# Performance work log

Hardware: AMD Instinct MI355X
Metric: run time of the kernel (lower is better)

The kernel has to match this reference:

```python
import jax, jax.numpy as jnp
import numpy as np

HID = 768
HEADS = 12
HEAD_LEN = HID // HEADS
SCALE_INV = 1.0 / np.sqrt(HEAD_LEN).astype(np.float32)


def setup_inputs() -> dict:
    key = jax.random.key(0)
    ks = jax.random.split(key, 5)
    std = 1.0 / np.sqrt(HID)
    return {
        "x": jax.random.normal(ks[0], (1, 4096, HID), dtype=jnp.float32),
        "w_q": jax.random.normal(ks[1], (HID, HID), dtype=jnp.float32) * std,
        "w_k": jax.random.normal(ks[2], (HID, HID), dtype=jnp.float32) * std,
        "w_v": jax.random.normal(ks[3], (HID, HID), dtype=jnp.float32) * std,
        "w_fc": jax.random.normal(ks[4], (HID, HID), dtype=jnp.float32) * std,
    }


def reference(x, w_q, w_k, w_v, w_fc):
    B, S, D = x.shape
    # torch Linear weight layout [out, in]: y = x @ W.T
    def proj_heads(w):
        y = jnp.einsum("bsd,ed->bse", x, w)
        return y.reshape(B, S, HEADS, HEAD_LEN).transpose(0, 2, 1, 3)  # bhsd
    q = proj_heads(w_q)
    k = proj_heads(w_k)
    v = proj_heads(w_v)
    scores = SCALE_INV * jnp.einsum("bhqd,bhkd->bhqk", q, k)
    attn = jax.nn.softmax(scores, axis=-1)
    out = jnp.einsum("bhqk,bhkd->bhqd", attn, v)
    out = out.transpose(0, 2, 1, 3).reshape(B, S, D)
    return jnp.einsum("bsd,ed->bse", out, w_fc)
```

## Files before the change

kernel.cpp:

```cpp
#include <hip/hip_runtime.h>
#include <hip/hip_bf16.h>

#define S_LEN 4096
#define HID 768
#define NHEAD 12
#define HL 64
#define PSS 72
#define QB 128

typedef __attribute__((ext_vector_type(8))) short short8;
typedef __attribute__((ext_vector_type(4))) float f32x4;
using bf16 = __hip_bfloat16;

__device__ __forceinline__ void gl2lds16(const void* g, void* l) {
  __builtin_amdgcn_global_load_lds((__attribute__((address_space(1))) void*)(g),
                                   (__attribute__((address_space(3))) void*)(l),
                                   16, 0, 0);
}

__device__ __forceinline__ f32x4 mfma_bf16(short8 a, short8 b, f32x4 c) {
  return __builtin_amdgcn_mfma_f32_16x16x32_bf16(a, b, c, 0, 0, 0);
}

__device__ __forceinline__ void storeC(float* C, long idx, float v) { C[idx] = v; }
__device__ __forceinline__ void storeC(bf16* C, long idx, float v) { C[idx] = __float2bfloat16(v); }

#define BAR() asm volatile("s_waitcnt lgkmcnt(0)\n\ts_barrier" ::: "memory")

__global__ __launch_bounds__(256) void cvt_all(
    const float* __restrict__ x, const float* __restrict__ wq,
    const float* __restrict__ wk, const float* __restrict__ wv,
    const float* __restrict__ wfc, bf16* __restrict__ xb, bf16* __restrict__ wqb,
    bf16* __restrict__ wkb, bf16* __restrict__ wvb, bf16* __restrict__ wfcb) {
  const long NX = (long)S_LEN * HID;
  const long NW = (long)HID * HID;
  long i = ((long)blockIdx.x * 256 + threadIdx.x) * 4;
  const float* src;
  bf16* dst;
  long off;
  if (i < NX) {
    src = x; dst = xb; off = i;
  } else {
    long j = i - NX;
    int wsel = (int)(j / NW);
    off = j - (long)wsel * NW;
    src = wsel == 0 ? wq : wsel == 1 ? wk : wsel == 2 ? wv : wfc;
    dst = wsel == 0 ? wqb : wsel == 1 ? wkb : wsel == 2 ? wvb : wfcb;
  }
  float4 v = *(const float4*)(src + off);
  bf16 h0 = __float2bfloat16(v.x), h1 = __float2bfloat16(v.y);
  bf16 h2 = __float2bfloat16(v.z), h3 = __float2bfloat16(v.w);
  ushort4 o;
  o.x = *(unsigned short*)&h0; o.y = *(unsigned short*)&h1;
  o.z = *(unsigned short*)&h2; o.w = *(unsigned short*)&h3;
  *(ushort4*)(dst + off) = o;
}

template <typename OT>
__global__ __launch_bounds__(256) void gemm_bt(
    const bf16* __restrict__ A, const bf16* __restrict__ B0,
    const bf16* __restrict__ B1, const bf16* __restrict__ B2,
    OT* __restrict__ C0, OT* __restrict__ C1, OT* __restrict__ C2, float qscale) {
  constexpr int K = HID;
  __shared__ __align__(16) bf16 As[128 * 32];
  __shared__ __align__(16) bf16 Bs[128 * 32];
  const int z = blockIdx.z;
  const bf16* B = (z == 0) ? B0 : (z == 1) ? B1 : B2;
  OT* C = (z == 0) ? C0 : (z == 1) ? C1 : C2;
  const float sc = (z == 0) ? qscale : 1.0f;
  const int bm = blockIdx.y, bn = blockIdx.x;
  const int t = threadIdx.x, lane = t & 63, w = t >> 6;
  const int wm = w >> 1, wn = w & 1;
  const int q4 = lane >> 4, c16 = lane & 15;
  const int srow = lane >> 2, scol = (lane & 3) * 8;
  const bf16* Ab = A + (long)bm * 128 * K;
  const bf16* Bb = B + (long)bn * 128 * K;
  f32x4 acc[4][4] = {};
  for (int k0 = 0; k0 < K; k0 += 32) {
#pragma unroll
    for (int r = 0; r < 2; ++r) {
      int rowb = r * 64 + w * 16;
      gl2lds16(Ab + (long)(rowb + srow) * K + k0 + scol, &As[rowb * 32]);
      gl2lds16(Bb + (long)(rowb + srow) * K + k0 + scol, &Bs[rowb * 32]);
    }
    __syncthreads();
    short8 af[4], bfv[4];
#pragma unroll
    for (int i = 0; i < 4; ++i)
      af[i] = *(const short8*)&As[(wm * 64 + i * 16 + c16) * 32 + q4 * 8];
#pragma unroll
    for (int j = 0; j < 4; ++j)
      bfv[j] = *(const short8*)&Bs[(wn * 64 + j * 16 + c16) * 32 + q4 * 8];
#pragma unroll
    for (int i = 0; i < 4; ++i)
#pragma unroll
      for (int j = 0; j < 4; ++j)
        acc[i][j] = mfma_bf16(af[i], bfv[j], acc[i][j]);
    __syncthreads();
  }
  const long crow0 = (long)bm * 128 + wm * 64;
  const int ccol0 = bn * 128 + wn * 64;
#pragma unroll
  for (int i = 0; i < 4; ++i)
#pragma unroll
    for (int j = 0; j < 4; ++j)
#pragma unroll
      for (int r = 0; r < 4; ++r) {
        long row = crow0 + i * 16 + q4 * 4 + r;
        int col = ccol0 + j * 16 + c16;
        storeC(C, row * HID + col, sc * acc[i][j][r]);
      }
}

__global__ __launch_bounds__(256) void gemm_fc(const bf16* __restrict__ A,
                                               const bf16* __restrict__ B,
                                               float* __restrict__ C) {
  __shared__ __align__(16) bf16 As[128 * 32];
  __shared__ __align__(16) bf16 Bs[64 * 32];
  const int bm = blockIdx.y, bn = blockIdx.x;
  const int t = threadIdx.x, lane = t & 63, w = t >> 6;
  const int q4 = lane >> 4, c16 = lane & 15;
  const int srow = lane >> 2, scol = (lane & 3) * 8;
  const bf16* Ab = A + (long)bm * 128 * HID;
  const bf16* Bb = B + (long)bn * 64 * HID;
  f32x4 acc[2][4] = {};
  for (int k0 = 0; k0 < HID; k0 += 32) {
#pragma unroll
    for (int r = 0; r < 2; ++r) {
      int rowb = w * 32 + r * 16;
      gl2lds16(Ab + (long)(rowb + srow) * HID + k0 + scol, &As[rowb * 32]);
    }
    gl2lds16(Bb + (long)(w * 16 + srow) * HID + k0 + scol, &Bs[w * 16 * 32]);
    __syncthreads();
    short8 af[2], bfv[4];
#pragma unroll
    for (int i = 0; i < 2; ++i)
      af[i] = *(const short8*)&As[(w * 32 + i * 16 + c16) * 32 + q4 * 8];
#pragma unroll
    for (int j = 0; j < 4; ++j)
      bfv[j] = *(const short8*)&Bs[(j * 16 + c16) * 32 + q4 * 8];
#pragma unroll
    for (int i = 0; i < 2; ++i)
#pragma unroll
      for (int j = 0; j < 4; ++j)
        acc[i][j] = mfma_bf16(af[i], bfv[j], acc[i][j]);
    __syncthreads();
  }
#pragma unroll
  for (int i = 0; i < 2; ++i)
#pragma unroll
    for (int j = 0; j < 4; ++j)
#pragma unroll
      for (int r = 0; r < 4; ++r) {
        long row = (long)bm * 128 + w * 32 + i * 16 + q4 * 4 + r;
        int col = bn * 64 + j * 16 + c16;
        C[row * HID + col] = acc[i][j][r];
      }
}

__global__ __launch_bounds__(256) void transpose_v(const bf16* __restrict__ V,
                                                   bf16* __restrict__ Vt) {
  __shared__ unsigned short tile[64][65];
  const int bs = blockIdx.x * 64;
  const int be = blockIdx.y * 64;
  const int t = threadIdx.x;
#pragma unroll
  for (int p = 0; p < 4; ++p) {
    int i = p * 256 + t;
    int r = i >> 4;
    int c = (i & 15) * 4;
    ushort4 v = *(const ushort4*)((const unsigned short*)V + (long)(bs + r) * HID + be + c);
    tile[r][c] = v.x; tile[r][c + 1] = v.y; tile[r][c + 2] = v.z; tile[r][c + 3] = v.w;
  }
  __syncthreads();
#pragma unroll
  for (int p = 0; p < 4; ++p) {
    int i = p * 256 + t;
    int r = i >> 4;
    int c = (i & 15) * 4;
    ushort4 v;
    v.x = tile[c][r]; v.y = tile[c + 1][r]; v.z = tile[c + 2][r]; v.w = tile[c + 3][r];
    *(ushort4*)((unsigned short*)Vt + (long)(be + r) * S_LEN + bs + c) = v;
  }
}

__global__ __launch_bounds__(256, 2) void flash_attn(const bf16* __restrict__ Q,
                                                     const bf16* __restrict__ Kg,
                                                     const bf16* __restrict__ Vt,
                                                     bf16* __restrict__ O) {
  __shared__ __align__(16) bf16 Ps[2][QB * PSS];
  __shared__ float Lred[4][QB];
  const int i0 = blockIdx.x;
  const int xcd = i0 & 7, sb = i0 >> 3;
  const int pair = xcd >> 1;
  const int r2 = sb * 2 + (xcd & 1);
  const int h = pair * 3 + (r2 >> 5);
  const int qt = r2 & 31;
  const int t = threadIdx.x, lane = t & 63, w = t >> 6;
  const int q4 = lane >> 4, c16 = lane & 15;
  const int s0 = qt * QB;

  short8 qf[2][8];
  {
    const bf16* Qb = Q + (long)(s0 + c16) * HID + h * HL + q4 * 8;
#pragma unroll
    for (int j = 0; j < 8; ++j)
#pragma unroll
      for (int ks = 0; ks < 2; ++ks)
        qf[ks][j] = *(const short8*)(Qb + (long)j * 16 * HID + ks * 32);
  }
  const bf16* kp = Kg + (long)(w * 16 + c16) * HID + h * HL + q4 * 8;
  const bf16* vp = Vt + (long)(h * HL + w * 16 + c16) * S_LEN + q4 * 8;

  float l_part[8] = {};
  f32x4 o_acc[8] = {};

  short8 kf0 = *(const short8*)(kp), kf1 = *(const short8*)(kp + 32);
  short8 vf0 = *(const short8*)(vp), vf1 = *(const short8*)(vp + 32);

  {
    f32x4 sacc[8] = {};
#pragma unroll
    for (int j = 0; j < 8; ++j) sacc[j] = mfma_bf16(kf0, qf[0][j], sacc[j]);
#pragma unroll
    for (int j = 0; j < 8; ++j) sacc[j] = mfma_bf16(kf1, qf[1][j], sacc[j]);
    kp += 64 * HID;
    kf0 = *(const short8*)(kp); kf1 = *(const short8*)(kp + 32);
#pragma unroll
    for (int j = 0; j < 8; ++j) {
      float p0 = __builtin_amdgcn_exp2f(sacc[j][0]);
      float p1 = __builtin_amdgcn_exp2f(sacc[j][1]);
      float p2 = __builtin_amdgcn_exp2f(sacc[j][2]);
      float p3 = __builtin_amdgcn_exp2f(sacc[j][3]);
      l_part[j] += (p0 + p1) + (p2 + p3);
      bf16 b0 = __float2bfloat16(p0), b1 = __float2bfloat16(p1);
      bf16 b2 = __float2bfloat16(p2), b3 = __float2bfloat16(p3);
      short4 pk;
      pk.x = *(short*)&b0; pk.y = *(short*)&b1; pk.z = *(short*)&b2; pk.w = *(short*)&b3;
      *(short4*)&Ps[0][(j * 16 + c16) * PSS + w * 16 + q4 * 4] = pk;
    }
  }
  BAR();

  constexpr int NT = S_LEN / 64;
  for (int kt = 0; kt < NT - 1; ++kt) {
    const int cur = kt & 1, nxt = cur ^ 1;
    const bf16* kpn = (kt + 2 < NT) ? kp + 64 * HID : kp;
    const bf16* vpn = vp + 64;
    short8 nk0 = *(const short8*)(kpn), nk1 = *(const short8*)(kpn + 32);
    short8 nv0 = *(const short8*)(vpn), nv1 = *(const short8*)(vpn + 32);

    f32x4 sacc[8] = {};
#pragma unroll
    for (int j = 0; j < 8; ++j) sacc[j] = mfma_bf16(kf0, qf[0][j], sacc[j]);
#pragma unroll
    for (int j = 0; j < 8; ++j) sacc[j] = mfma_bf16(kf1, qf[1][j], sacc[j]);

#pragma unroll
    for (int ks = 0; ks < 2; ++ks) {
      short8 vfk = ks ? vf1 : vf0;
#pragma unroll
      for (int j = 0; j < 8; ++j) {
        short8 pf = *(const short8*)&Ps[cur][(j * 16 + c16) * PSS + ks * 32 + q4 * 8];
        o_acc[j] = mfma_bf16(vfk, pf, o_acc[j]);
      }
    }

#pragma unroll
    for (int j = 0; j < 8; ++j) {
      float p0 = __builtin_amdgcn_exp2f(sacc[j][0]);
      float p1 = __builtin_amdgcn_exp2f(sacc[j][1]);
      float p2 = __builtin_amdgcn_exp2f(sacc[j][2]);
      float p3 = __builtin_amdgcn_exp2f(sacc[j][3]);
      l_part[j] += (p0 + p1) + (p2 + p3);
      bf16 b0 = __float2bfloat16(p0), b1 = __float2bfloat16(p1);
      bf16 b2 = __float2bfloat16(p2), b3 = __float2bfloat16(p3);
      short4 pk;
      pk.x = *(short*)&b0; pk.y = *(short*)&b1; pk.z = *(short*)&b2; pk.w = *(short*)&b3;
      *(short4*)&Ps[nxt][(j * 16 + c16) * PSS + w * 16 + q4 * 4] = pk;
    }

    BAR();
    kf0 = nk0; kf1 = nk1; vf0 = nv0; vf1 = nv1;
    kp = kpn; vp = vpn;
  }

  {
    const int cur = (NT - 1) & 1;
#pragma unroll
    for (int ks = 0; ks < 2; ++ks) {
      short8 vfk = ks ? vf1 : vf0;
#pragma unroll
      for (int j = 0; j < 8; ++j) {
        short8 pf = *(const short8*)&Ps[cur][(j * 16 + c16) * PSS + ks * 32 + q4 * 8];
        o_acc[j] = mfma_bf16(vfk, pf, o_acc[j]);
      }
    }
  }

#pragma unroll
  for (int j = 0; j < 8; ++j) {
    float s = l_part[j];
    s += __shfl_xor(s, 16, 64);
    s += __shfl_xor(s, 32, 64);
    Lred[w][j * 16 + c16] = s;
  }
  BAR();
#pragma unroll
  for (int j = 0; j < 8; ++j) {
    int q = j * 16 + c16;
    float lt = (Lred[0][q] + Lred[1][q]) + (Lred[2][q] + Lred[3][q]);
    float rl = 1.0f / lt;
    float v0 = o_acc[j][0] * rl, v1 = o_acc[j][1] * rl;
    float v2 = o_acc[j][2] * rl, v3 = o_acc[j][3] * rl;
    bf16 b0 = __float2bfloat16(v0), b1 = __float2bfloat16(v1);
    bf16 b2 = __float2bfloat16(v2), b3 = __float2bfloat16(v3);
    short4 pk;
    pk.x = *(short*)&b0; pk.y = *(short*)&b1; pk.z = *(short*)&b2; pk.w = *(short*)&b3;
    *(short4*)&O[(long)(s0 + q) * HID + h * HL + w * 16 + q4 * 4] = pk;
  }
}

extern "C" void kernel_launch(void* const* d_in, const int* in_sizes, int n_in,
                              void* d_out, int out_size, void* d_ws, size_t ws_size,
                              hipStream_t stream) {
  const float* x = (const float*)d_in[0];
  const float* wq = (const float*)d_in[1];
  const float* wk = (const float*)d_in[2];
  const float* wv = (const float*)d_in[3];
  const float* wfc = (const float*)d_in[4];
  float* out = (float*)d_out;

  const long NBIG = (long)S_LEN * HID * sizeof(bf16);
  const long NWB = (long)HID * HID * sizeof(bf16);
  char* p = (char*)d_ws;
  bf16* xb = (bf16*)p;   p += NBIG;
  bf16* wqb = (bf16*)p;  p += NWB;
  bf16* wkb = (bf16*)p;  p += NWB;
  bf16* wvb = (bf16*)p;  p += NWB;
  bf16* wfcb = (bf16*)p; p += NWB;
  bf16* Qb = (bf16*)p;   p += NBIG;
  bf16* Kb = (bf16*)p;   p += NBIG;
  bf16* Vb = (bf16*)p;   p += NBIG;
  bf16* Vtb = (bf16*)p;  p += NBIG;
  bf16* Ob = (bf16*)p;   p += NBIG;

  const float c1 = 0.125f * 1.44269504088896340736f;

  const long total4 = ((long)S_LEN * HID + 4L * HID * HID) / 4;
  cvt_all<<<(int)(total4 / 256), 256, 0, stream>>>(x, wq, wk, wv, wfc, xb, wqb, wkb,
                                                   wvb, wfcb);
  gemm_bt<bf16><<<dim3(HID / 128, S_LEN / 128, 3), 256, 0, stream>>>(
      xb, wqb, wkb, wvb, Qb, Kb, Vb, c1);
  transpose_v<<<dim3(S_LEN / 64, HID / 64), 256, 0, stream>>>(Vb, Vtb);
  flash_attn<<<dim3(S_LEN / QB * NHEAD), 256, 0, stream>>>(Qb, Kb, Vtb, Ob);
  gemm_fc<<<dim3(HID / 64, S_LEN / 128), 256, 0, stream>>>(Ob, wfcb, out);
}
```

Measured before the change: 210.9 us.

## Split attention key range in two halves and combine partial outputs

Splits each attention block's key sequence into two halves processed by separate blocks, doubling the grid from 384 to 768 blocks to fill more compute units. Each half writes unnormalised fp32 partial outputs and row sums, and a new combine kernel adds them and normalises to bf16. Launch bounds are raised to 3 blocks per SIMD. The trade is extra fp32 global traffic, an additional kernel launch, and tighter register limits that may cause spills.

```diff
diff --git a/kernel.cpp b/kernel.cpp
--- a/kernel.cpp
+++ b/kernel.cpp
@@ -184,21 +184,25 @@
   }
 }
 
-__global__ __launch_bounds__(256, 2) void flash_attn(const bf16* __restrict__ Q,
+__global__ __launch_bounds__(256, 3) void flash_attn(const bf16* __restrict__ Q,
                                                      const bf16* __restrict__ Kg,
                                                      const bf16* __restrict__ Vt,
-                                                     bf16* __restrict__ O) {
+                                                     float* __restrict__ Opart,
+                                                     float* __restrict__ Lpart) {
   __shared__ __align__(16) bf16 Ps[2][QB * PSS];
   __shared__ float Lred[4][QB];
   const int i0 = blockIdx.x;
   const int xcd = i0 & 7, sb = i0 >> 3;
   const int pair = xcd >> 1;
   const int r2 = sb * 2 + (xcd & 1);
-  const int h = pair * 3 + (r2 >> 5);
-  const int qt = r2 & 31;
+  const int h = pair * 3 + (r2 >> 6);
+  const int rem = r2 & 63;
+  const int qt = rem >> 1;
+  const int g = rem & 1;
   const int t = threadIdx.x, lane = t & 63, w = t >> 6;
   const int q4 = lane >> 4, c16 = lane & 15;
   const int s0 = qt * QB;
+  constexpr int NTH = S_LEN / 64 / 2;
 
   short8 qf[2][8];
   {
@@ -209,8 +213,8 @@
       for (int ks = 0; ks < 2; ++ks)
         qf[ks][j] = *(const short8*)(Qb + (long)j * 16 * HID + ks * 32);
   }
-  const bf16* kp = Kg + (long)(w * 16 + c16) * HID + h * HL + q4 * 8;
-  const bf16* vp = Vt + (long)(h * HL + w * 16 + c16) * S_LEN + q4 * 8;
+  const bf16* kp = Kg + (long)(g * NTH * 64 + w * 16 + c16) * HID + h * HL + q4 * 8;
+  const bf16* vp = Vt + (long)(h * HL + w * 16 + c16) * S_LEN + g * NTH * 64 + q4 * 8;
 
   float l_part[8] = {};
   f32x4 o_acc[8] = {};
@@ -242,10 +246,9 @@
   }
   BAR();
 
-  constexpr int NT = S_LEN / 64;
-  for (int kt = 0; kt < NT - 1; ++kt) {
+  for (int kt = 0; kt < NTH - 1; ++kt) {
     const int cur = kt & 1, nxt = cur ^ 1;
-    const bf16* kpn = (kt + 2 < NT) ? kp + 64 * HID : kp;
+    const bf16* kpn = (kt + 2 < NTH) ? kp + 64 * HID : kp;
     const bf16* vpn = vp + 64;
     short8 nk0 = *(const short8*)(kpn), nk1 = *(const short8*)(kpn + 32);
     short8 nv0 = *(const short8*)(vpn), nv1 = *(const short8*)(vpn + 32);
@@ -286,7 +289,7 @@
   }
 
   {
-    const int cur = (NT - 1) & 1;
+    const int cur = (NTH - 1) & 1;
 #pragma unroll
     for (int ks = 0; ks < 2; ++ks) {
       short8 vfk = ks ? vf1 : vf0;
@@ -306,19 +309,44 @@
     Lred[w][j * 16 + c16] = s;
   }
   BAR();
+  if (w == 0 && q4 == 0) {
+#pragma unroll
+    for (int j = 0; j < 8; ++j) {
+      int q = j * 16 + c16;
+      float lt = (Lred[0][q] + Lred[1][q]) + (Lred[2][q] + Lred[3][q]);
+      Lpart[((long)g * NHEAD + h) * S_LEN + s0 + q] = lt;
+    }
+  }
 #pragma unroll
   for (int j = 0; j < 8; ++j) {
     int q = j * 16 + c16;
-    float lt = (Lred[0][q] + Lred[1][q]) + (Lred[2][q] + Lred[3][q]);
-    float rl = 1.0f / lt;
-    float v0 = o_acc[j][0] * rl, v1 = o_acc[j][1] * rl;
-    float v2 = o_acc[j][2] * rl, v3 = o_acc[j][3] * rl;
-    bf16 b0 = __float2bfloat16(v0), b1 = __float2bfloat16(v1);
-    bf16 b2 = __float2bfloat16(v2), b3 = __float2bfloat16(v3);
-    short4 pk;
-    pk.x = *(short*)&b0; pk.y = *(short*)&b1; pk.z = *(short*)&b2; pk.w = *(short*)&b3;
-    *(short4*)&O[(long)(s0 + q) * HID + h * HL + w * 16 + q4 * 4] = pk;
-  }
+    *(f32x4*)&Opart[((long)g * S_LEN + s0 + q) * HID + h * HL + w * 16 + q4 * 4] =
+        o_acc[j];
+  }
+}
+
+__global__ __launch_bounds__(256) void combine_o(const float* __restrict__ Opart,
+                                                 const float* __restrict__ Lpart,
+                                                 bf16* __restrict__ O) {
+  const long NTOT = (long)S_LEN * HID;
+  long flat = ((long)blockIdx.x * 256 + threadIdx.x) * 4;
+  if (flat >= NTOT) return;
+  int q = (int)(flat / HID);
+  int col = (int)(flat - (long)q * HID);
+  int h = col >> 6;
+  float4 a = *(const float4*)(Opart + flat);
+  float4 b = *(const float4*)(Opart + NTOT + flat);
+  float l0 = Lpart[(long)h * S_LEN + q];
+  float l1 = Lpart[(long)NHEAD * S_LEN + (long)h * S_LEN + q];
+  float rl = 1.0f / (l0 + l1);
+  bf16 o0 = __float2bfloat16((a.x + b.x) * rl);
+  bf16 o1 = __float2bfloat16((a.y + b.y) * rl);
+  bf16 o2 = __float2bfloat16((a.z + b.z) * rl);
+  bf16 o3 = __float2bfloat16((a.w + b.w) * rl);
+  ushort4 pk;
+  pk.x = *(unsigned short*)&o0; pk.y = *(unsigned short*)&o1;
+  pk.z = *(unsigned short*)&o2; pk.w = *(unsigned short*)&o3;
+  *(ushort4*)((unsigned short*)O + flat) = pk;
 }
 
 extern "C" void kernel_launch(void* const* d_in, const int* in_sizes, int n_in,
@@ -333,17 +361,20 @@
 
   const long NBIG = (long)S_LEN * HID * sizeof(bf16);
   const long NWB = (long)HID * HID * sizeof(bf16);
+  const long NOF = (long)S_LEN * HID * sizeof(float);
   char* p = (char*)d_ws;
-  bf16* xb = (bf16*)p;   p += NBIG;
-  bf16* wqb = (bf16*)p;  p += NWB;
-  bf16* wkb = (bf16*)p;  p += NWB;
-  bf16* wvb = (bf16*)p;  p += NWB;
-  bf16* wfcb = (bf16*)p; p += NWB;
-  bf16* Qb = (bf16*)p;   p += NBIG;
-  bf16* Kb = (bf16*)p;   p += NBIG;
-  bf16* Vb = (bf16*)p;   p += NBIG;
-  bf16* Vtb = (bf16*)p;  p += NBIG;
-  bf16* Ob = (bf16*)p;   p += NBIG;
+  bf16* xb = (bf16*)p;    p += NBIG;
+  bf16* wqb = (bf16*)p;   p += NWB;
+  bf16* wkb = (bf16*)p;   p += NWB;
+  bf16* wvb = (bf16*)p;   p += NWB;
+  bf16* wfcb = (bf16*)p;  p += NWB;
+  bf16* Qb = (bf16*)p;    p += NBIG;
+  bf16* Kb = (bf16*)p;    p += NBIG;
+  bf16* Vb = (bf16*)p;    p += NBIG;
+  bf16* Vtb = (bf16*)p;   p += NBIG;
+  bf16* Ob = (bf16*)p;    p += NBIG;
+  float* Opart = (float*)p; p += 2 * NOF;
+  float* Lpart = (float*)p; p += 2L * NHEAD * S_LEN * sizeof(float);
 
   const float c1 = 0.125f * 1.44269504088896340736f;
 
@@ -353,6 +384,9 @@
   gemm_bt<bf16><<<dim3(HID / 128, S_LEN / 128, 3), 256, 0, stream>>>(
       xb, wqb, wkb, wvb, Qb, Kb, Vb, c1);
   transpose_v<<<dim3(S_LEN / 64, HID / 64), 256, 0, stream>>>(Vb, Vtb);
-  flash_attn<<<dim3(S_LEN / QB * NHEAD), 256, 0, stream>>>(Qb, Kb, Vtb, Ob);
+  flash_attn<<<dim3(S_LEN / QB * NHEAD * 2), 256, 0, stream>>>(Qb, Kb, Vtb, Opart,
+                                                               Lpart);
+  combine_o<<<(int)(((long)S_LEN * HID / 4 + 255) / 256), 256, 0, stream>>>(
+      Opart, Lpart, Ob);
   gemm_fc<<<dim3(HID / 64, S_LEN / 128), 256, 0, stream>>>(Ob, wfcb, out);
 }
```

Result: slower. 226.4 us (+7.4%).
